# Kernel optimization log

Hardware: AMD Instinct MI355X
Metric: run time of the kernel (lower is better)

## Reference

```python
import jax, jax.numpy as jnp
import numpy as np

E = 2048        # embed_dim
H = 16          # num_heads
D = 128         # head_dim
K = 4           # num_hyper_nodes (timelines)
N = 4096        # seq_len
B = 1           # batch (module asserts batch==1)
CAP_FACTOR = 1.25
CAP = int(N / K * CAP_FACTOR)   # 1280, static
ROPE_BASE = 10000.0
SCALE = D ** -0.5
NEG_INF = jnp.float32(-1e30)


def setup_inputs() -> dict:
    key = jax.random.key(0)
    ks = jax.random.split(key, 10)
    def xavier(k, shape):
        fan_in, fan_out = shape[0], shape[1]
        lim = np.sqrt(6.0 / (fan_in + fan_out))
        return jax.random.uniform(k, shape, jnp.float32, -lim, lim)
    return {
        'x':   jax.random.normal(ks[0], (B, N, E), jnp.float32),
        # weights stored (in, out); equivalent to torch Linear weight.T
        'Wq':  xavier(ks[1], (E, H * D)),
        'Wk':  xavier(ks[2], (E, H * D)),
        'Wv':  xavier(ks[3], (E, H * D)),
        'Wo':  xavier(ks[4], (H * D, E)),
        'Wr1': xavier(ks[5], (E, E // 2)),
        'br1': jnp.zeros((E // 2,), jnp.float32),
        'Wr2': xavier(ks[6], (E // 2, K)),
        'br2': jnp.zeros((K,), jnp.float32),
    }


def _rope_tables():
    # local positions: arange(CAP) (use_local_rope=True)
    inv_freq = 1.0 / (ROPE_BASE ** (jnp.arange(0, D, 2, dtype=jnp.float32) / D))
    freqs = jnp.arange(CAP, dtype=jnp.float32)[:, None] * inv_freq[None, :]  # (CAP, D/2)
    emb = jnp.concatenate([freqs, freqs], axis=-1)  # (CAP, D)
    return jnp.cos(emb), jnp.sin(emb)


def _rotate_half(t):
    return jnp.concatenate([-t[..., D // 2:], t[..., :D // 2]], axis=-1)


def reference(x, Wq, Wk, Wv, Wo, Wr1, br1, Wr2, br2):
    # --- expert-choice routing ---
    h = jax.nn.gelu(x @ Wr1 + br1, approximate=False)      # (B, N, E/2)
    scores = h @ Wr2 + br2                                  # (B, N, K)
    scores_t = scores[0].T                                  # (K, N)
    topk_scores, topk_idx = jax.lax.top_k(scores_t, CAP)    # (K, CAP)
    sel_w = jax.nn.softmax(topk_scores, axis=-1)            # (K, CAP)
    aux_loss = -jnp.mean(jnp.max(scores, axis=-1))

    # --- projections ---
    q = (x @ Wq).reshape(B, N, H, D).transpose(0, 2, 1, 3)  # (B, H, N, D)
    k = (x @ Wk).reshape(B, N, H, D).transpose(0, 2, 1, 3)
    v = (x @ Wv).reshape(B, N, H, D).transpose(0, 2, 1, 3)

    cos, sin = _rope_tables()                               # (CAP, D)
    causal = jnp.tril(jnp.ones((CAP, CAP), bool))

    def timeline(idx, w):
        # gather this timeline's tokens
        qt = q[:, :, idx]                                   # (B, H, CAP, D)
        kt = k[:, :, idx]
        vt = v[:, :, idx]
        qt = qt * cos + _rotate_half(qt) * sin
        kt = kt * cos + _rotate_half(kt) * sin
        att = jnp.einsum('bhqd,bhkd->bhqk', qt, kt) * SCALE
        att = jnp.where(causal, att, NEG_INF)
        att = jax.nn.softmax(att, axis=-1)
        o = jnp.einsum('bhqk,bhkd->bhqd', att, vt)          # (B, H, CAP, D)
        return o * w[None, None, :, None]                   # weighted combine

    outs = jax.vmap(timeline)(topk_idx, sel_w)              # (K, B, H, CAP, D)

    # scatter back: sum contributions over timelines
    idx_flat = topk_idx.reshape(-1)                         # (K*CAP,)
    vals = outs.transpose(1, 2, 0, 3, 4).reshape(B, H, K * CAP, D)
    out = jnp.zeros((B, H, N, D), x.dtype).at[:, :, idx_flat, :].add(vals)

    out = out.transpose(0, 2, 1, 3).reshape(B, N, H * D) @ Wo  # (B, N, E)
    return out, aux_loss
```

## Files before the change

kernel.cpp:

```cpp
#include <hip/hip_runtime.h>
#include <cstdint>
#include <cstddef>

#define N_TOK 4096
#define E_DIM 2048
#define NH    16
#define DH    128
#define KEXP  4
#define CAPN  1280
#define NTILE 20
#define NQB   10
#define QKV_STRIDE 6144
#define SCALE_QK 0.08838834764831845f
#define LOG2E    1.4426950408889634f
#define NEG_BIG -1e30f

typedef __attribute__((ext_vector_type(4))) float f32x4;
typedef __attribute__((ext_vector_type(8))) short s16x8;

__device__ __forceinline__ float bf2f(unsigned short u){
  union{unsigned int i; float fl;} c; c.i = ((unsigned int)u)<<16; return c.fl;
}
__device__ __forceinline__ unsigned short f2bf(float x){
  union{float fl; unsigned int i;} c; c.fl=x;
  return (unsigned short)((c.i + 0x7FFFu + ((c.i>>16)&1u))>>16);
}
__device__ __forceinline__ f32x4 mfma_bf16(s16x8 a, s16x8 b, f32x4 c){
  asm("v_mfma_f32_16x16x32_bf16 %0, %1, %2, %0" : "+v"(c) : "v"(a), "v"(b));
  return c;
}
__device__ __forceinline__ void gl_lds16(const unsigned short* g, unsigned short* l){
  __builtin_amdgcn_global_load_lds(
      (const __attribute__((address_space(1))) unsigned int*)g,
      (__attribute__((address_space(3))) unsigned int*)l, 16, 0, 0);
}

__global__ __launch_bounds__(256) void conv_x_kernel(const float* __restrict__ x,
    unsigned short* __restrict__ hi, unsigned short* __restrict__ lo, int n4){
  int idx = blockIdx.x*256 + threadIdx.x;
  if (idx >= n4) return;
  float4 v = ((const float4*)x)[idx];
  float ar[4] = {v.x, v.y, v.z, v.w};
  union{ unsigned short u[4]; uint2 q; } H, L;
  #pragma unroll
  for(int i=0;i<4;i++){
    unsigned short h = f2bf(ar[i]);
    H.u[i] = h;
    L.u[i] = f2bf(ar[i] - bf2f(h));
  }
  ((uint2*)hi)[idx] = H.q;
  ((uint2*)lo)[idx] = L.q;
}

__global__ __launch_bounds__(256) void tconv_kernel(const float* __restrict__ W,
    unsigned short* __restrict__ Thi, unsigned short* __restrict__ Tlo, int R, int C){
  __shared__ float t[32][33];
  int tx = threadIdx.x, ty = threadIdx.y;
  int c0 = blockIdx.x*32, r0 = blockIdx.y*32;
  #pragma unroll
  for(int i=0;i<4;i++){
    int r = r0 + ty + i*8;
    t[ty+i*8][tx] = W[(size_t)r*C + c0 + tx];
  }
  __syncthreads();
  #pragma unroll
  for(int i=0;i<4;i++){
    int c = c0 + ty + i*8;
    float v = t[tx][ty+i*8];
    size_t o = (size_t)c*R + r0 + tx;
    unsigned short h = f2bf(v);
    Thi[o] = h;
    if (Tlo) Tlo[o] = f2bf(v - bf2f(h));
  }
}

__global__ __launch_bounds__(256) void tconv4_kernel(const float* __restrict__ W0,
    const float* __restrict__ W1, const float* __restrict__ W2, const float* __restrict__ W3,
    unsigned short* __restrict__ out){
  __shared__ float t[32][33];
  int z = blockIdx.z;
  const float* W = (z==0)?W0 : (z==1)?W1 : (z==2)?W2 : W3;
  unsigned short* T = out + (size_t)z*E_DIM*E_DIM;
  int tx = threadIdx.x, ty = threadIdx.y;
  int c0 = blockIdx.x*32, r0 = blockIdx.y*32;
  #pragma unroll
  for(int i=0;i<4;i++){
    int r = r0 + ty + i*8;
    t[ty+i*8][tx] = W[(size_t)r*E_DIM + c0 + tx];
  }
  __syncthreads();
  #pragma unroll
  for(int i=0;i<4;i++){
    int c = c0 + ty + i*8;
    T[(size_t)c*E_DIM + r0 + tx] = f2bf(t[tx][ty+i*8]);
  }
}

template<int OUTBF>
__global__ __launch_bounds__(512, 2) void gemm_p(
    const unsigned short* __restrict__ A, const unsigned short* __restrict__ Bt,
    void* __restrict__ Cp, int N, int Kd){
  __shared__ __align__(16) unsigned short lds[3*12288];
  const int tid = threadIdx.x;
  const int w = tid>>6, lane = tid&63, g = lane>>4, r16 = lane&15;
  const int wm = w>>2, wn = w&3;
  const int mb = blockIdx.y, nb = blockIdx.x;
  const unsigned short* Ab = A  + (size_t)mb*128*Kd;
  const unsigned short* Bb = Bt + (size_t)nb*256*Kd;
  const int PMAX = Kd >> 5;

  f32x4 acc[4][4];
  #pragma unroll
  for(int i=0;i<4;i++)
    #pragma unroll
    for(int j=0;j<4;j++) acc[i][j] = f32x4{0.f,0.f,0.f,0.f};

  auto stageP = [&](int Pst, int slot){
    unsigned short* base = &lds[slot*12288];
    const int col = Pst*32;
    {
      int row = tid>>2, ch = tid&3;
      int sc = ch ^ ((row>>1)&3);
      gl_lds16(Ab + (size_t)row*Kd + col + sc*8, base + tid*8);
    }
    #pragma unroll
    for(int i=0;i<2;i++){
      int n = i*512 + tid;
      int rw = n>>2, c2 = n&3;
      int s2 = c2 ^ ((rw>>1)&3);
      gl_lds16(Bb + (size_t)rw*Kd + col + s2*8, base + 4096 + n*8);
    }
  };
  const int xoff = (g ^ ((r16>>1)&3)) << 3;

  stageP(0,0); stageP(1,1);
  asm volatile("s_waitcnt vmcnt(3)" ::: "memory");
  __builtin_amdgcn_s_barrier();

  int sR = 0, sW = 2;
  for(int P=0; P<PMAX; ++P){
    const unsigned short* base = &lds[sR*12288];
    s16x8 af[4], bfv[4];
    #pragma unroll
    for(int mf=0;mf<4;mf++)
      af[mf] = *(const s16x8*)&base[(wm*64 + mf*16 + r16)*32 + xoff];
    #pragma unroll
    for(int nf=0;nf<4;nf++)
      bfv[nf] = *(const s16x8*)&base[4096 + (wn*64 + nf*16 + r16)*32 + xoff];
    if (P+2 < PMAX) stageP(P+2, sW);
    __builtin_amdgcn_s_setprio(1);
    #pragma unroll
    for(int mf=0;mf<4;mf++)
      #pragma unroll
      for(int nf=0;nf<4;nf++)
        acc[mf][nf] = mfma_bf16(af[mf], bfv[nf], acc[mf][nf]);
    __builtin_amdgcn_s_setprio(0);
    if      (P+2 < PMAX) asm volatile("s_waitcnt vmcnt(3)" ::: "memory");
    else                 asm volatile("s_waitcnt vmcnt(0)" ::: "memory");
    __builtin_amdgcn_s_barrier();
    sR = (sR==2) ? 0 : sR+1;
    sW = (sW==2) ? 0 : sW+1;
  }

  const int rowb = mb*128 + wm*64, colb = nb*256 + wn*64;
  #pragma unroll
  for(int mf=0;mf<4;mf++)
    #pragma unroll
    for(int nf=0;nf<4;nf++)
      #pragma unroll
      for(int r=0;r<4;r++){
        int rr = rowb + mf*16 + 4*g + r;
        int cc = colb + nf*16 + r16;
        size_t o = (size_t)rr*N + cc;
        if (OUTBF) ((unsigned short*)Cp)[o] = f2bf(acc[mf][nf][r]);
        else       ((float*)Cp)[o] = acc[mf][nf][r];
      }
}

__global__ __launch_bounds__(256, 2) void gemm_router_p(
    const unsigned short* __restrict__ Ahi, const unsigned short* __restrict__ Alo,
    const unsigned short* __restrict__ Bhi, const unsigned short* __restrict__ Blo,
    const float* __restrict__ br1, float* __restrict__ H){
  __shared__ __align__(16) unsigned short lds[3*12288];
  const int tid = threadIdx.x;
  const int w = tid>>6, lane = tid&63, g = lane>>4, r16 = lane&15;
  const int mb = blockIdx.y, nb = blockIdx.x;
  const unsigned short* AbH = Ahi + (size_t)mb*64*E_DIM;
  const unsigned short* AbL = Alo + (size_t)mb*64*E_DIM;
  const unsigned short* BbH = Bhi + (size_t)nb*128*E_DIM;
  const unsigned short* BbL = Blo + (size_t)nb*128*E_DIM;
  const int PMAX = E_DIM >> 5;

  f32x4 acc[4][2];
  #pragma unroll
  for(int i=0;i<4;i++){ acc[i][0]=f32x4{0.f,0.f,0.f,0.f}; acc[i][1]=f32x4{0.f,0.f,0.f,0.f}; }

  auto stageP = [&](int Pst, int slot){
    unsigned short* base = &lds[slot*12288];
    const int col = Pst*32;
    {
      int row = tid>>2, ch = tid&3;
      int sc = ch ^ ((row>>1)&3);
      size_t go = (size_t)row*E_DIM + col + sc*8;
      gl_lds16(AbH + go, base +        tid*8);
      gl_lds16(AbL + go, base + 2048 + tid*8);
    }
    #pragma unroll
    for(int i=0;i<2;i++){
      int n = i*256 + tid;
      int row = n>>2, ch = n&3;
      int sc = ch ^ ((row>>1)&3);
      size_t go = (size_t)row*E_DIM + col + sc*8;
      gl_lds16(BbH + go, base + 4096 + n*8);
      gl_lds16(BbL + go, base + 8192 + n*8);
    }
  };
  const int xoff = (g ^ ((r16>>1)&3)) << 3;

  stageP(0,0); stageP(1,1);
  asm volatile("s_waitcnt vmcnt(6)" ::: "memory");
  __builtin_amdgcn_s_barrier();

  int sR = 0, sW = 2;
  for(int P=0; P<PMAX; ++P){
    const unsigned short* base = &lds[sR*12288];
    s16x8 ah[4], al[4], bh[2], bl[2];
    #pragma unroll
    for(int mf=0;mf<4;mf++){
      int ro = (mf*16 + r16)*32 + xoff;
      ah[mf] = *(const s16x8*)&base[ro];
      al[mf] = *(const s16x8*)&base[2048 + ro];
    }
    #pragma unroll
    for(int nf=0;nf<2;nf++){
      int rb = (w*32 + nf*16 + r16)*32 + xoff;
      bh[nf] = *(const s16x8*)&base[4096 + rb];
      bl[nf] = *(const s16x8*)&base[8192 + rb];
    }
    if (P+2 < PMAX) stageP(P+2, sW);
    __builtin_amdgcn_s_setprio(1);
    #pragma unroll
    for(int mf=0;mf<4;mf++)
      #pragma unroll
      for(int nf=0;nf<2;nf++){
        acc[mf][nf] = mfma_bf16(ah[mf], bh[nf], acc[mf][nf]);
        acc[mf][nf] = mfma_bf16(ah[mf], bl[nf], acc[mf][nf]);
        acc[mf][nf] = mfma_bf16(al[mf], bh[nf], acc[mf][nf]);
      }
    __builtin_amdgcn_s_setprio(0);
    if      (P+2 < PMAX) asm volatile("s_waitcnt vmcnt(6)" ::: "memory");
    else                 asm volatile("s_waitcnt vmcnt(0)" ::: "memory");
    __builtin_amdgcn_s_barrier();
    sR = (sR==2) ? 0 : sR+1;
    sW = (sW==2) ? 0 : sW+1;
  }

  const int rowb = mb*64, colb = nb*128 + w*32;
  #pragma unroll
  for(int mf=0;mf<4;mf++)
    #pragma unroll
    for(int nf=0;nf<2;nf++)
      #pragma unroll
      for(int r=0;r<4;r++){
        int rr = rowb + mf*16 + 4*g + r;
        int cc = colb + nf*16 + r16;
        float v = acc[mf][nf][r] + br1[cc];
        H[(size_t)rr*1024 + cc] = 0.5f*v*(1.0f + erff(v*0.70710678118654752f));
      }
}

__global__ __launch_bounds__(256) void scores_kernel(const float* __restrict__ h,
    const float* __restrict__ Wr2, const float* __restrict__ br2,
    float* __restrict__ scores, float* __restrict__ tokmax){
  int tid = threadIdx.x;
  int n = blockIdx.x*4 + (tid>>6);
  int lane = tid & 63;
  const float* hr = h + (size_t)n*1024;
  float s0=0,s1=0,s2=0,s3=0;
  #pragma unroll
  for(int i=0;i<16;i++){
    int j = lane + i*64;
    float hv = hr[j];
    float4 wv = *(const float4*)(Wr2 + (size_t)j*4);
    s0 += hv*wv.x; s1 += hv*wv.y; s2 += hv*wv.z; s3 += hv*wv.w;
  }
  #pragma unroll
  for(int m=32;m>=1;m>>=1){
    s0 += __shfl_xor(s0,m); s1 += __shfl_xor(s1,m);
    s2 += __shfl_xor(s2,m); s3 += __shfl_xor(s3,m);
  }
  if (lane==0){
    s0+=br2[0]; s1+=br2[1]; s2+=br2[2]; s3+=br2[3];
    scores[n*4+0]=s0; scores[n*4+1]=s1; scores[n*4+2]=s2; scores[n*4+3]=s3;
    tokmax[n]=fmaxf(fmaxf(s0,s1),fmaxf(s2,s3));
  }
}

__global__ __launch_bounds__(1024) void aux_kernel(const float* __restrict__ tokmax, float* __restrict__ out_aux){
  __shared__ float red[1024];
  int t = threadIdx.x;
  red[t] = tokmax[t] + tokmax[t+1024] + tokmax[t+2048] + tokmax[t+3072];
  __syncthreads();
  for(int k=512;k>=1;k>>=1){ if(t<k) red[t]+=red[t+k]; __syncthreads(); }
  if (t==0) out_aux[0] = -red[0]/4096.0f;
}

__global__ __launch_bounds__(256) void rank_kernel(const float* __restrict__ scores,
    int* __restrict__ topk_idx, float* __restrict__ topv, int* __restrict__ rank_of){
  __shared__ unsigned long long keys[4096];
  const int e = blockIdx.y, blk = blockIdx.x, tid = threadIdx.x;
  for(int i=tid;i<4096;i+=256){
    unsigned u = __float_as_uint(scores[i*4+e]);
    unsigned m = (u & 0x80000000u) ? ~u : (u | 0x80000000u);
    keys[i] = (((unsigned long long)m)<<32) | (unsigned)(4095-i);
  }
  __syncthreads();
  const int i = blk*256 + tid;
  const unsigned long long mykey = keys[i];
  int cnt = 0;
  #pragma unroll 8
  for(int j=0;j<4096;j++) cnt += (keys[j] > mykey) ? 1 : 0;
  if (cnt < CAPN){
    topk_idx[e*CAPN + cnt] = i;
    topv[e*CAPN + cnt]     = scores[i*4+e];
    rank_of[e*4096 + i]    = cnt;
  } else {
    rank_of[e*4096 + i]    = -1;
  }
}

__global__ __launch_bounds__(1024) void selw_kernel(const float* __restrict__ topv,
    float* __restrict__ sel_w){
  __shared__ float red[1024];
  const int e = blockIdx.x, t = threadIdx.x;
  const float mx = topv[e*CAPN];
  float p0 = expf(topv[e*CAPN + t] - mx);
  float p1 = (t + 1024 < CAPN) ? expf(topv[e*CAPN + t + 1024] - mx) : 0.f;
  red[t] = p0 + p1;
  __syncthreads();
  for(int k=512;k>=1;k>>=1){ if(t<k) red[t]+=red[t+k]; __syncthreads(); }
  const float denom = red[0];
  sel_w[e*CAPN + t] = p0/denom;
  if (t + 1024 < CAPN) sel_w[e*CAPN + t + 1024] = p1/denom;
}

__global__ __launch_bounds__(256) void rope_kernel(float* __restrict__ cosT, float* __restrict__ sinT){
  int idx = blockIdx.x*256 + threadIdx.x;
  int p = idx>>6, dm = idx&63;
  float inv = powf(10000.0f, -(float)dm/64.0f);
  float ang = (float)p*inv;
  cosT[idx]=cosf(ang);
  sinT[idx]=sinf(ang);
}

__global__ __launch_bounds__(256) void prerope_k_kernel(const unsigned short* __restrict__ kb,
    const int* __restrict__ topk_idx, const float* __restrict__ cosT, const float* __restrict__ sinT,
    unsigned short* __restrict__ Kg){
  int idx = blockIdx.x*256 + threadIdx.x;
  int ch = idx & 15;
  int rest = idx >> 4;
  int rank = rest % CAPN;
  int he = rest / CAPN;
  int e = he >> 4, h = he & 15;
  int tok = topk_idx[e*CAPN + rank];
  int d0 = ch*8;
  const unsigned short* krow = kb + (size_t)tok*QKV_STRIDE + h*DH;
  unsigned short held[8], part[8];
  *(uint4*)held = *(const uint4*)(krow + d0);
  *(uint4*)part = *(const uint4*)(krow + (d0^64));
  const float* cr = cosT + rank*64;
  const float* sr = sinT + rank*64;
  float sgn = (d0<64) ? -1.f : 1.f;
  unsigned short outv[8];
  #pragma unroll
  for(int jj=0;jj<8;jj++){
    int dm = (d0+jj)&63;
    outv[jj] = f2bf(bf2f(held[jj])*cr[dm] + sgn*bf2f(part[jj])*sr[dm]);
  }
  int t = rank >> 6, row = rank & 63;
  size_t tbase = ((size_t)(he)*NTILE + t) * 8192;
  *(uint4*)(Kg + tbase + row*128 + ((ch ^ (row&7))<<3)) = *(uint4*)outv;
}

__global__ __launch_bounds__(256) void prev_kernel(const unsigned short* __restrict__ vb,
    const int* __restrict__ topk_idx, unsigned short* __restrict__ Vg){
  __shared__ __align__(16) unsigned short T2[128][72];
  int bid = blockIdx.x;
  int t = bid % NTILE, h = (bid/NTILE) & 15, e = bid/(NTILE*NH);
  int tid = threadIdx.x, lane = tid & 63, dchb = tid >> 6;
  int tok = topk_idx[e*CAPN + t*64 + lane];
  const unsigned short* vrow = vb + (size_t)tok*QKV_STRIDE + h*DH;
  #pragma unroll
  for(int i=0;i<4;i++){
    int d0 = (dchb + i*4)*8;
    unsigned short vv[8];
    *(uint4*)vv = *(const uint4*)(vrow + d0);
    #pragma unroll
    for(int j=0;j<8;j++) T2[d0+j][lane] = vv[j];
  }
  __syncthreads();
  unsigned short* out = Vg + ((size_t)(e*NH+h)*NTILE + t)*8192;
  #pragma unroll
  for(int i=0;i<4;i++){
    int c = i*256 + tid;
    int d = c>>3, ch = c&7;
    *(uint4*)(out + d*64 + ((ch ^ (d&7))<<3)) = *(const uint4*)&T2[d][ch*8];
  }
}

__global__ __launch_bounds__(512) void attn_kernel(
    const unsigned short* __restrict__ qb,
    const unsigned short* __restrict__ Kg, const unsigned short* __restrict__ Vg,
    const int* __restrict__ topk_idx, const float* __restrict__ sel_w,
    const float* __restrict__ cosT, const float* __restrict__ sinT,
    unsigned short* __restrict__ oexp){
  __shared__ __align__(16) unsigned short KsA[2][8192];
  __shared__ __align__(16) unsigned short Vs[8192];
  __shared__ __align__(16) unsigned short Ps[8][16][72];
  const int id = blockIdx.x;
  const int xcd = id & 7, s_ = id >> 3;
  const int qb2 = NQB - 1 - (s_ % NQB);
  const int grp = (s_ / NQB)*8 + xcd;
  const int e = grp >> 4, hh = grp & 15;
  const int tid = threadIdx.x, w = tid>>6, lane = tid&63, g = lane>>4, r16 = lane&15;
  const int* idxE = topk_idx + e*CAPN;
  const unsigned short* Kgb = Kg + (size_t)(e*NH+hh)*CAPN*DH;
  const unsigned short* Vgb = Vg + (size_t)(e*NH+hh)*CAPN*DH;
  const int ktmax = 2*qb2 + 1;

  s16x8 aq[4];
  {
    int qr = qb2*128 + w*16 + r16;
    int tok = idxE[qr];
    const unsigned short* qrow = qb + (size_t)tok*QKV_STRIDE + hh*DH;
    const float* cr = cosT + qr*64;
    const float* sr = sinT + qr*64;
    #pragma unroll
    for(int s=0;s<4;s++){
      int d0 = s*32 + 8*g;
      unsigned short held[8], part[8];
      *(uint4*)held = *(const uint4*)(qrow + d0);
      *(uint4*)part = *(const uint4*)(qrow + (d0^64));
      float sgn = (d0<64) ? -1.f : 1.f;
      union{ s16x8 v; unsigned short u[8]; } fr;
      #pragma unroll
      for(int jj=0;jj<8;jj++){
        int dm = (d0+jj)&63;
        float val = bf2f(held[jj])*cr[dm] + sgn*bf2f(part[jj])*sr[dm];
        fr.u[jj] = f2bf(val * (SCALE_QK*LOG2E));
      }
      aq[s] = fr.v;
    }
  }
  float m_r[4], l_r[4];
  f32x4 o[8];
  #pragma unroll
  for(int r=0;r<4;r++){ m_r[r]=-INFINITY; l_r[r]=0.f; }
  #pragma unroll
  for(int f2=0;f2<8;f2++) o[f2]=f32x4{0.f,0.f,0.f,0.f};

  #pragma unroll
  for(int i=0;i<2;i++){ int c=i*512+tid; gl_lds16(Kgb + c*8, &KsA[0][c*8]); }
  #pragma unroll
  for(int i=0;i<2;i++){ int c=i*512+tid; gl_lds16(Vgb + c*8, &Vs[c*8]); }
  asm volatile("s_waitcnt vmcnt(2)" ::: "memory");
  __builtin_amdgcn_s_barrier();

  for(int kt=0; kt<=ktmax; kt++){
    const int cur = kt & 1;
    if (kt < ktmax){
      const unsigned short* Ksrc = Kgb + (size_t)(kt+1)*8192;
      #pragma unroll
      for(int i=0;i<2;i++){ int c=i*512+tid; gl_lds16(Ksrc + c*8, &KsA[cur^1][c*8]); }
    }
    f32x4 sfr[4];
    #pragma unroll
    for(int fc=0;fc<4;fc++){
      f32x4 a4 = f32x4{0.f,0.f,0.f,0.f};
      const int row = fc*16 + r16;
      #pragma unroll
      for(int s=0;s<4;s++){
        s16x8 bk = *(const s16x8*)&KsA[cur][row*128 + (((s*4+g) ^ (r16&7))<<3)];
        a4 = mfma_bf16(aq[s], bk, a4);
      }
      sfr[fc] = a4;
    }
    if (kt >= 2*qb2){
      #pragma unroll
      for(int fc=0;fc<4;fc++)
        #pragma unroll
        for(int r=0;r<4;r++){
          int qrank  = qb2*128 + w*16 + 4*g + r;
          int kvrank = kt*64 + fc*16 + r16;
          if (kvrank > qrank) sfr[fc][r] = NEG_BIG;
        }
    }
    float corr[4];
    bool need = false;
    #pragma unroll
    for(int r=0;r<4;r++){
      float mx = fmaxf(fmaxf(sfr[0][r],sfr[1][r]), fmaxf(sfr[2][r],sfr[3][r]));
      #pragma unroll
      for(int mk=1;mk<16;mk<<=1) mx = fmaxf(mx, __shfl_xor(mx,mk));
      float nm = fmaxf(m_r[r], mx);
      need = need || (nm > m_r[r]);
      corr[r] = exp2f(m_r[r]-nm);
      m_r[r] = nm;
    }
    if (__any(need)){
      #pragma unroll
      for(int f2=0;f2<8;f2++)
        #pragma unroll
        for(int r=0;r<4;r++) o[f2][r] *= corr[r];
      #pragma unroll
      for(int r=0;r<4;r++) l_r[r] *= corr[r];
    }
    float rs[4] = {0.f,0.f,0.f,0.f};
    #pragma unroll
    for(int fc=0;fc<4;fc++)
      #pragma unroll
      for(int r=0;r<4;r++){
        float p = exp2f(sfr[fc][r] - m_r[r]);
        rs[r] += p;
        Ps[w][4*g+r][fc*16+r16] = f2bf(p);
      }
    #pragma unroll
    for(int r=0;r<4;r++){
      float ts = rs[r];
      #pragma unroll
      for(int mk=1;mk<16;mk<<=1) ts += __shfl_xor(ts,mk);
      l_r[r] += ts;
    }
    if (kt < ktmax) asm volatile("s_waitcnt vmcnt(2)" ::: "memory");
    else            asm volatile("s_waitcnt vmcnt(0)" ::: "memory");
    __builtin_amdgcn_s_barrier();
    #pragma unroll
    for(int ks=0;ks<2;ks++){
      s16x8 pa = *(const s16x8*)&Ps[w][r16][ks*32 + 8*g];
      #pragma unroll
      for(int fd=0;fd<8;fd++){
        const int row = fd*16 + r16;
        s16x8 vf = *(const s16x8*)&Vs[row*64 + (((ks*4+g) ^ (r16&7))<<3)];
        o[fd] = mfma_bf16(pa, vf, o[fd]);
      }
    }
    __builtin_amdgcn_s_barrier();
    if (kt < ktmax){
      const unsigned short* Vsrc = Vgb + (size_t)(kt+1)*8192;
      #pragma unroll
      for(int i=0;i<2;i++){ int c=i*512+tid; gl_lds16(Vsrc + c*8, &Vs[c*8]); }
      asm volatile("s_waitcnt vmcnt(2)" ::: "memory");
      __builtin_amdgcn_s_barrier();
    }
  }
  #pragma unroll
  for(int r=0;r<4;r++){
    int qrank = qb2*128 + w*16 + 4*g + r;
    float fac = sel_w[e*CAPN + qrank] / l_r[r];
    #pragma unroll
    for(int fd=0;fd<8;fd++){
      oexp[((size_t)(e*CAPN + qrank))*E_DIM + hh*DH + fd*16 + r16] = f2bf(o[fd][r]*fac);
    }
  }
}

__global__ __launch_bounds__(256) void acc_kernel(const unsigned short* __restrict__ oexp,
    const int* __restrict__ rank_of, unsigned short* __restrict__ accb){
  int n = blockIdx.x, t = threadIdx.x;
  int base = t*8;
  float s[8] = {0,0,0,0,0,0,0,0};
  #pragma unroll
  for(int e=0;e<4;e++){
    int r = rank_of[e*4096+n];
    if (r>=0){
      union{uint4 q; unsigned short u[8];} ld;
      ld.q = *(const uint4*)(oexp + ((size_t)(e*CAPN+r))*E_DIM + base);
      #pragma unroll
      for(int j2=0;j2<8;j2++) s[j2] += bf2f(ld.u[j2]);
    }
  }
  union{uint4 q; unsigned short u[8];} st;
  #pragma unroll
  for(int j2=0;j2<8;j2++) st.u[j2] = f2bf(s[j2]);
  *(uint4*)(accb + (size_t)n*E_DIM + base) = st.q;
}

extern "C" void kernel_launch(void* const* d_in, const int* in_sizes, int n_in,
                              void* d_out, int out_size, void* d_ws, size_t ws_size,
                              hipStream_t stream) {
  const float* x   = (const float*)d_in[0];
  const float* Wq  = (const float*)d_in[1];
  const float* Wk  = (const float*)d_in[2];
  const float* Wv  = (const float*)d_in[3];
  const float* Wo  = (const float*)d_in[4];
  const float* Wr1 = (const float*)d_in[5];
  const float* br1 = (const float*)d_in[6];
  const float* Wr2 = (const float*)d_in[7];
  const float* br2 = (const float*)d_in[8];

  char* ws = (char*)d_ws;
  size_t off = 0;
  auto alloc = [&](size_t bytes)->void*{
    void* p = ws + off;
    off += (bytes + 255) & ~(size_t)255;
    return p;
  };
  unsigned short* xhi   = (unsigned short*)alloc((size_t)N_TOK*E_DIM*2);
  unsigned short* xlo   = (unsigned short*)alloc((size_t)N_TOK*E_DIM*2);
  unsigned short* wr1hi = (unsigned short*)alloc((size_t)E_DIM*1024*2);
  unsigned short* wr1lo = (unsigned short*)alloc((size_t)E_DIM*1024*2);
  unsigned short* wqkvT = (unsigned short*)alloc((size_t)3*E_DIM*E_DIM*2);
  unsigned short* woT   = (unsigned short*)alloc((size_t)E_DIM*E_DIM*2);
  void* hv = alloc((size_t)KEXP*NH*CAPN*DH*2);
  float* hbuf = (float*)hv;
  unsigned short* Vg = (unsigned short*)hv;
  float* scores = (float*)alloc((size_t)N_TOK*4*4);
  float* tokmax = (float*)alloc((size_t)N_TOK*4);
  int*   topkI  = (int*)alloc((size_t)KEXP*CAPN*4);
  float* topv   = (float*)alloc((size_t)KEXP*CAPN*4);
  float* selw   = (float*)alloc((size_t)KEXP*CAPN*4);
  int*   rankof = (int*)alloc((size_t)KEXP*N_TOK*4);
  float* cosT   = (float*)alloc((size_t)CAPN*64*4);
  float* sinT   = (float*)alloc((size_t)CAPN*64*4);
  unsigned short* qkvbuf = (unsigned short*)alloc((size_t)N_TOK*QKV_STRIDE*2);
  unsigned short* oexp = (unsigned short*)alloc((size_t)KEXP*CAPN*E_DIM*2);
  unsigned short* accb = (unsigned short*)alloc((size_t)N_TOK*E_DIM*2);
  if (off > ws_size) return;

  unsigned short* Kg = xlo;

  conv_x_kernel<<<(N_TOK*E_DIM/4+255)/256, 256, 0, stream>>>(x, xhi, xlo, N_TOK*E_DIM/4);
  tconv_kernel<<<dim3(1024/32, E_DIM/32), dim3(32,8), 0, stream>>>(Wr1, wr1hi, wr1lo, E_DIM, 1024);
  tconv4_kernel<<<dim3(E_DIM/32, E_DIM/32, 4), dim3(32,8), 0, stream>>>(Wq, Wk, Wv, Wo, wqkvT);

  gemm_router_p<<<dim3(1024/128, N_TOK/64), 256, 0, stream>>>(xhi, xlo, wr1hi, wr1lo, br1, hbuf);
  scores_kernel<<<N_TOK/4, 256, 0, stream>>>(hbuf, Wr2, br2, scores, tokmax);
  aux_kernel<<<1, 1024, 0, stream>>>(tokmax, ((float*)d_out) + (size_t)N_TOK*E_DIM);
  rank_kernel<<<dim3(16, KEXP), 256, 0, stream>>>(scores, topkI, topv, rankof);
  selw_kernel<<<KEXP, 1024, 0, stream>>>(topv, selw);
  rope_kernel<<<CAPN*64/256, 256, 0, stream>>>(cosT, sinT);

  gemm_p<1><<<dim3(QKV_STRIDE/256, N_TOK/128), 512, 0, stream>>>(xhi, wqkvT, qkvbuf, QKV_STRIDE, E_DIM);

  prerope_k_kernel<<<KEXP*NH*CAPN*16/256, 256, 0, stream>>>(qkvbuf + E_DIM, topkI, cosT, sinT, Kg);
  prev_kernel<<<KEXP*NH*NTILE, 256, 0, stream>>>(qkvbuf + 2*E_DIM, topkI, Vg);

  attn_kernel<<<KEXP*NH*NQB, 512, 0, stream>>>(qkvbuf, Kg, Vg, topkI, selw, cosT, sinT, oexp);

  acc_kernel<<<N_TOK, 256, 0, stream>>>(oexp, rankof, accb);

  gemm_p<0><<<dim3(E_DIM/256, N_TOK/128), 512, 0, stream>>>(accb, woT, (float*)d_out, E_DIM, E_DIM);
}
```

Baseline: 439.6 us.

## Drop K double-buffering in attention, load K/V synchronously per tile, add MFMA priority

The attention kernel no longer prefetches the next K tile into a second LDS buffer or staggers V loads. It now loads K and V for the current tile, waits for them with vmcnt(0) and a barrier, and raises wave priority around the QK and PV MFMA blocks. This halves the LDS used for K, which may let more blocks fit per CU and removes several barriers. In exchange, global-load latency is no longer hidden within a block, and the kernel relies on other resident waves to cover it.

```diff
diff --git a/kernel.cpp b/kernel.cpp
--- a/kernel.cpp
+++ b/kernel.cpp
@@ -414,7 +414,7 @@
     const int* __restrict__ topk_idx, const float* __restrict__ sel_w,
     const float* __restrict__ cosT, const float* __restrict__ sinT,
     unsigned short* __restrict__ oexp){
-  __shared__ __align__(16) unsigned short KsA[2][8192];
+  __shared__ __align__(16) unsigned short Ks[8192];
   __shared__ __align__(16) unsigned short Vs[8192];
   __shared__ __align__(16) unsigned short Ps[8][16][72];
   const int id = blockIdx.x;
@@ -459,32 +459,31 @@
   #pragma unroll
   for(int f2=0;f2<8;f2++) o[f2]=f32x4{0.f,0.f,0.f,0.f};
 
-  #pragma unroll
-  for(int i=0;i<2;i++){ int c=i*512+tid; gl_lds16(Kgb + c*8, &KsA[0][c*8]); }
-  #pragma unroll
-  for(int i=0;i<2;i++){ int c=i*512+tid; gl_lds16(Vgb + c*8, &Vs[c*8]); }
-  asm volatile("s_waitcnt vmcnt(2)" ::: "memory");
-  __builtin_amdgcn_s_barrier();
-
   for(int kt=0; kt<=ktmax; kt++){
-    const int cur = kt & 1;
-    if (kt < ktmax){
-      const unsigned short* Ksrc = Kgb + (size_t)(kt+1)*8192;
-      #pragma unroll
-      for(int i=0;i<2;i++){ int c=i*512+tid; gl_lds16(Ksrc + c*8, &KsA[cur^1][c*8]); }
-    }
+    {
+      const unsigned short* Ksrc = Kgb + (size_t)kt*8192;
+      const unsigned short* Vsrc = Vgb + (size_t)kt*8192;
+      #pragma unroll
+      for(int i=0;i<2;i++){ int c=i*512+tid; gl_lds16(Ksrc + c*8, &Ks[c*8]); }
+      #pragma unroll
+      for(int i=0;i<2;i++){ int c=i*512+tid; gl_lds16(Vsrc + c*8, &Vs[c*8]); }
+    }
+    asm volatile("s_waitcnt vmcnt(0)" ::: "memory");
+    __builtin_amdgcn_s_barrier();
     f32x4 sfr[4];
+    __builtin_amdgcn_s_setprio(1);
     #pragma unroll
     for(int fc=0;fc<4;fc++){
       f32x4 a4 = f32x4{0.f,0.f,0.f,0.f};
       const int row = fc*16 + r16;
       #pragma unroll
       for(int s=0;s<4;s++){
-        s16x8 bk = *(const s16x8*)&KsA[cur][row*128 + (((s*4+g) ^ (r16&7))<<3)];
+        s16x8 bk = *(const s16x8*)&Ks[row*128 + (((s*4+g) ^ (r16&7))<<3)];
         a4 = mfma_bf16(aq[s], bk, a4);
       }
       sfr[fc] = a4;
     }
+    __builtin_amdgcn_s_setprio(0);
     if (kt >= 2*qb2){
       #pragma unroll
       for(int fc=0;fc<4;fc++)
@@ -531,9 +530,7 @@
       for(int mk=1;mk<16;mk<<=1) ts += __shfl_xor(ts,mk);
       l_r[r] += ts;
     }
-    if (kt < ktmax) asm volatile("s_waitcnt vmcnt(2)" ::: "memory");
-    else            asm volatile("s_waitcnt vmcnt(0)" ::: "memory");
-    __builtin_amdgcn_s_barrier();
+    __builtin_amdgcn_s_setprio(1);
     #pragma unroll
     for(int ks=0;ks<2;ks++){
       s16x8 pa = *(const s16x8*)&Ps[w][r16][ks*32 + 8*g];
@@ -544,14 +541,8 @@
         o[fd] = mfma_bf16(pa, vf, o[fd]);
       }
     }
-    __builtin_amdgcn_s_barrier();
-    if (kt < ktmax){
-      const unsigned short* Vsrc = Vgb + (size_t)(kt+1)*8192;
-      #pragma unroll
-      for(int i=0;i<2;i++){ int c=i*512+tid; gl_lds16(Vsrc + c*8, &Vs[c*8]); }
-      asm volatile("s_waitcnt vmcnt(2)" ::: "memory");
-      __builtin_amdgcn_s_barrier();
-    }
+    __builtin_amdgcn_s_setprio(0);
+    if (kt < ktmax) __builtin_amdgcn_s_barrier();
   }
   #pragma unroll
   for(int r=0;r<4;r++){
```

After: 444.3 us. About the same (+1.1%).
